# Kernel tuning notes

Hardware: AMD Instinct MI355X
Metric: run time of the kernel (lower is better)

The kernel has to match this reference:

```python
import jax, jax.numpy as jnp
import numpy as np

DIM = 10  # GMM components == feature dim


def _conv(x, w, b):
    y = jax.lax.conv_general_dilated(x, w, window_strides=(1, 1), padding='VALID',
                                     dimension_numbers=('NCHW', 'OIHW', 'NCHW'))
    return y + b[None, :, None, None]


def _gmm(x, centers, raw_mats):
    # x: [B, d]; centers: [K, d]; raw_mats: [K, d, d] with K == d == DIM
    K, d = centers.shape
    I = jnp.eye(d, dtype=x.dtype)
    L = jnp.tril(raw_mats, -1) + I                       # unit lower-triangular [K,d,d]
    root_D = jnp.diagonal(raw_mats, axis1=-2, axis2=-1)  # [K,d]
    D = root_D * root_D + 1e-4
    # Sigma_inv = L^{-T} D^{-1} L^{-1}
    L_inv = jax.scipy.linalg.solve_triangular(L, jnp.broadcast_to(I, L.shape), lower=True)
    Sigma_inv = jnp.einsum('kai,ka,kaj->kij', L_inv, 1.0 / D, L_inv)
    det_scale = jax.lax.rsqrt(jnp.prod(D, axis=-1))      # [K]
    diff = x[:, None, :] - centers[None, :, :]           # [B,K,d]
    dist_sq = jnp.einsum('bkd,kde,bke->bk', diff, Sigma_inv, diff)
    expo = -0.5 * dist_sq
    expo_safe = expo - jnp.max(expo, axis=1, keepdims=True)
    numer = det_scale[None, :] * jnp.exp(expo_safe)
    return numer / jnp.sum(numer, axis=1, keepdims=True)


def setup_inputs() -> dict:
    key = jax.random.key(0)
    ks = jax.random.split(key, 12)
    B = 4096
    x = jax.random.normal(ks[0], (B, 1, 28, 28), dtype=jnp.float32)
    conv1_w = jax.random.normal(ks[1], (32, 1, 3, 3), jnp.float32) * (1.0 / np.sqrt(1 * 9))
    conv1_b = jnp.zeros((32,), jnp.float32)
    conv2_w = jax.random.normal(ks[2], (64, 32, 3, 3), jnp.float32) * (1.0 / np.sqrt(32 * 9))
    conv2_b = jnp.zeros((64,), jnp.float32)
    fc1_w = jax.random.normal(ks[3], (128, 9216), jnp.float32) * (1.0 / np.sqrt(9216))
    fc1_b = jnp.zeros((128,), jnp.float32)
    fc2_w = jax.random.normal(ks[4], (DIM, 128), jnp.float32) * (1.0 / np.sqrt(128))
    fc2_b = jnp.zeros((DIM,), jnp.float32)
    centers = jax.random.normal(ks[5], (DIM, DIM), jnp.float32)
    raw_mats = jax.random.normal(ks[6], (DIM, DIM, DIM), jnp.float32) * 0.1 + jnp.eye(DIM)[None]
    return {'x': x, 'conv1_w': conv1_w, 'conv1_b': conv1_b, 'conv2_w': conv2_w,
            'conv2_b': conv2_b, 'fc1_w': fc1_w, 'fc1_b': fc1_b, 'fc2_w': fc2_w,
            'fc2_b': fc2_b, 'centers': centers, 'raw_mats': raw_mats}


def reference(x, conv1_w, conv1_b, conv2_w, conv2_b, fc1_w, fc1_b, fc2_w, fc2_b, centers, raw_mats):
    h = jax.nn.relu(_conv(x, conv1_w, conv1_b))          # [B,32,26,26]
    h = jax.nn.relu(_conv(h, conv2_w, conv2_b))          # [B,64,24,24]
    h = jax.lax.reduce_window(h, -jnp.inf, jax.lax.max, (1, 1, 2, 2), (1, 1, 2, 2), 'VALID')
    h = h.reshape(h.shape[0], -1)                        # [B,9216] (dropout = identity in eval)
    h = jax.nn.relu(h @ fc1_w.T + fc1_b)
    h = h @ fc2_w.T + fc2_b                              # [B,10]
    return _gmm(h, centers, raw_mats)
```

## Files before the change

### kernel.cpp

```cpp
#include <hip/hip_runtime.h>

typedef _Float16 half_t;
typedef _Float16 half8  __attribute__((ext_vector_type(8)));
typedef _Float16 half2v __attribute__((ext_vector_type(2)));
typedef float    floatx4 __attribute__((ext_vector_type(4)));

#define MFMA16(a, b, c) __builtin_amdgcn_mfma_f32_16x16x32_f16((a), (b), (c), 0, 0, 0)

__global__ void k_prep(const float* __restrict__ fw1, half_t* __restrict__ W1h,
                       const float* __restrict__ w2, half_t* __restrict__ W2T,
                       const float* __restrict__ raw, float* __restrict__ Sinv,
                       float* __restrict__ dets) {
    const int blk = blockIdx.x;
    const int t = threadIdx.x;
    if (blk < 4608) {
        const int i = blk * 256 + t;
        W1h[i] = (half_t)fw1[i];
    } else if (blk < 4680) {
        const int i = (blk - 4608) * 256 + t;
        if (i < 18432) {
            const int tap = i / 2048;
            const int r = i - tap * 2048;
            const int co = r >> 5;
            const int ci = r & 31;
            W2T[i] = (half_t)w2[(co * 32 + ci) * 9 + tap];
        }
    } else if (t < 10) {
        const float* R = raw + t * 100;
        float Rr[100];
#pragma unroll
        for (int i = 0; i < 100; ++i) Rr[i] = R[i];
        float Li[10][10];
#pragma unroll
        for (int j = 0; j < 10; ++j) {
#pragma unroll
            for (int i = 0; i < 10; ++i) Li[i][j] = (i == j) ? 1.0f : 0.0f;
#pragma unroll
            for (int i = 1; i < 10; ++i) {
                if (i > j) {
                    float s = 0.0f;
#pragma unroll
                    for (int m = 0; m < 10; ++m)
                        if (m >= j && m < i) s -= Rr[i * 10 + m] * Li[m][j];
                    Li[i][j] = s;
                }
            }
        }
        float Dl[10];
        float prod = 1.0f;
#pragma unroll
        for (int a = 0; a < 10; ++a) {
            float rd = Rr[a * 10 + a];
            float dv = rd * rd + 1e-4f;
            Dl[a] = 1.0f / dv;
            prod *= dv;
        }
        dets[t] = rsqrtf(prod);
#pragma unroll
        for (int i = 0; i < 10; ++i)
#pragma unroll
            for (int j = 0; j < 10; ++j) {
                float s = 0.0f;
#pragma unroll
                for (int a = 0; a < 10; ++a) s += Li[a][i] * Dl[a] * Li[a][j];
                Sinv[t * 100 + i * 10 + j] = s;
            }
    }
}

__global__ __launch_bounds__(256, 2) void k_convs(
    const float* __restrict__ x, const float* __restrict__ w1,
    const float* __restrict__ b1, const float* __restrict__ b2,
    const half_t* __restrict__ W2T, half_t* __restrict__ h2p) {
    __shared__ float s_x[784];
    __shared__ float s_w1[288];
    __shared__ float s_b1[32];
    __shared__ float s_b2[64];
    __shared__ __align__(16) half_t s_h1[4][26][26][8];

    const int t = threadIdx.x;
    const int b = blockIdx.x;

    for (int i = t; i < 784; i += 256) s_x[i] = x[(size_t)b * 784 + i];
    for (int i = t; i < 288; i += 256) s_w1[i] = w1[i];
    if (t < 32) s_b1[t] = b1[t];
    if (t < 64) s_b2[t] = b2[t];
    __syncthreads();

    const int w = t >> 6;
    const int ln = t & 63;
    const int n16 = ln & 15;
    const int q = ln >> 4;

    {
        float wr[8][9], br[8];
#pragma unroll
        for (int j = 0; j < 8; ++j) {
            br[j] = s_b1[w * 8 + j];
#pragma unroll
            for (int k = 0; k < 9; ++k) wr[j][k] = s_w1[(w * 8 + j) * 9 + k];
        }
        for (int p = ln; p < 676; p += 64) {
            const int yy = p / 26;
            const int xx = p - yy * 26;
            float win[9];
#pragma unroll
            for (int r = 0; r < 3; ++r)
#pragma unroll
                for (int c = 0; c < 3; ++c) win[r * 3 + c] = s_x[(yy + r) * 28 + xx + c];
            half8 hv;
#pragma unroll
            for (int j = 0; j < 8; ++j) {
                float a = br[j];
#pragma unroll
                for (int k = 0; k < 9; ++k) a = fmaf(win[k], wr[j][k], a);
                hv[j] = (half_t)fmaxf(a, 0.0f);
            }
            *(half8*)(&s_h1[w][yy][xx][0]) = hv;
        }
    }

    half8 bf[9][4];
#pragma unroll
    for (int tap = 0; tap < 9; ++tap)
#pragma unroll
        for (int ct = 0; ct < 4; ++ct)
            bf[tap][ct] = *(const half8*)(W2T + ((tap * 64 + ct * 16 + n16) * 32 + q * 8));

    __syncthreads();

#pragma unroll
    for (int tap = 0; tap < 9; ++tap)
#pragma unroll
        for (int ct = 0; ct < 4; ++ct)
            asm volatile("" : "+v"(bf[tap][ct]));

    const int dy = (ln >> 3) & 1;
    const int dx = ln & 7;

    for (int i = 0; i < 9; ++i) {
        const int mt = w * 9 + i;
        const int ty = mt / 3;
        const int tx = mt - ty * 3;
        const int y0 = 2 * ty, x0 = 8 * tx;
        floatx4 acc[4];
#pragma unroll
        for (int ct = 0; ct < 4; ++ct) acc[ct] = (floatx4){0.f, 0.f, 0.f, 0.f};
#pragma unroll
        for (int tap = 0; tap < 9; ++tap) {
            const int ky = tap / 3;
            const int kx = tap - ky * 3;
            half8 af = *(const half8*)(&s_h1[q][y0 + dy + ky][x0 + dx + kx][0]);
#pragma unroll
            for (int ct = 0; ct < 4; ++ct) acc[ct] = MFMA16(af, bf[tap][ct], acc[ct]);
        }
#pragma unroll
        for (int ct = 0; ct < 4; ++ct) {
            float p0 = fmaxf(acc[ct][0], acc[ct][1]);
            float p1 = fmaxf(acc[ct][2], acc[ct][3]);
            p0 = fmaxf(p0, __shfl_xor(p0, 32, 64));
            p1 = fmaxf(p1, __shfl_xor(p1, 32, 64));
            if (q < 2) {
                const int co = ct * 16 + n16;
                const float bb = s_b2[co];
                half2v hz;
                hz[0] = (half_t)fmaxf(p0 + bb, 0.0f);
                hz[1] = (half_t)fmaxf(p1 + bb, 0.0f);
                *(half2v*)(h2p + (size_t)b * 9216 + co * 144 + ty * 12 + 4 * tx + 2 * q) = hz;
            }
        }
    }
}

__global__ __launch_bounds__(256) void k_fc1(const half_t* __restrict__ A,
                                             const half_t* __restrict__ W,
                                             half_t* __restrict__ part) {
    const int t = threadIdx.x;
    const int mb = blockIdx.x;
    const int kb = blockIdx.y;
    const int w = t >> 6, ln = t & 63, n16 = ln & 15, q = ln >> 4;

    const half_t* a0 = A + (size_t)(mb * 128 + w * 32 + n16) * 9216 + kb * 576 + q * 8;
    const half_t* a1 = a0 + (size_t)16 * 9216;
    const half_t* wp = W + (size_t)n16 * 9216 + kb * 576 + q * 8;

    floatx4 acc[2][8];
#pragma unroll
    for (int s = 0; s < 2; ++s)
#pragma unroll
        for (int nt = 0; nt < 8; ++nt) acc[s][nt] = (floatx4){0.f, 0.f, 0.f, 0.f};

    for (int kt = 0; kt < 18; ++kt) {
        const int ko = kt * 32;
        half8 af0 = *(const half8*)(a0 + ko);
        half8 af1 = *(const half8*)(a1 + ko);
#pragma unroll
        for (int nt = 0; nt < 8; ++nt) {
            half8 bfr = *(const half8*)(wp + (size_t)nt * 16 * 9216 + ko);
            acc[0][nt] = MFMA16(af0, bfr, acc[0][nt]);
            acc[1][nt] = MFMA16(af1, bfr, acc[1][nt]);
        }
    }
    const int rowbase = mb * 128 + w * 32;
#pragma unroll
    for (int s = 0; s < 2; ++s)
#pragma unroll
        for (int nt = 0; nt < 8; ++nt)
#pragma unroll
            for (int r = 0; r < 4; ++r) {
                const int row = rowbase + s * 16 + q * 4 + r;
                const int col = nt * 16 + n16;
                part[(size_t)kb * 524288 + (size_t)row * 128 + col] = (half_t)acc[s][nt][r];
            }
}

__global__ void k_fc1red(const half_t* __restrict__ part, const float* __restrict__ b,
                         half_t* __restrict__ h3) {
    const int idx = blockIdx.x * 256 + threadIdx.x;
    const int col = idx & 127;
    float s = 0.0f;
#pragma unroll
    for (int j = 0; j < 16; ++j) s += (float)part[(size_t)j * 524288 + idx];
    s = fmaxf(s + b[col], 0.0f);
    h3[idx] = (half_t)s;
}

__global__ __launch_bounds__(256) void k_fc2gmm(
    const half_t* __restrict__ h3, const float* __restrict__ fw,
    const float* __restrict__ fb, const float* __restrict__ cent,
    const float* __restrict__ Sinv, const float* __restrict__ dets,
    float* __restrict__ out) {
    __shared__ float sw[1280];
    __shared__ float sb[10];
    __shared__ float sc[100];
    __shared__ float ss[1000];
    __shared__ float sd[10];
    const int t = threadIdx.x;
    for (int i = t; i < 1280; i += 256) sw[i] = fw[i];
    if (t < 10) sb[t] = fb[t];
    if (t < 100) sc[t] = cent[t];
    for (int i = t; i < 1000; i += 256) ss[i] = Sinv[i];
    if (t < 10) sd[t] = dets[t];
    __syncthreads();

    const int bidx = blockIdx.x * 256 + t;
    half2v hh[64];
    const half2v* hp = (const half2v*)(h3 + (size_t)bidx * 128);
#pragma unroll
    for (int i = 0; i < 64; ++i) hh[i] = hp[i];

    float y[10];
#pragma unroll
    for (int o = 0; o < 10; ++o) {
        float a = sb[o];
#pragma unroll
        for (int k = 0; k < 64; ++k) {
            a = fmaf((float)hh[k][0], sw[o * 128 + 2 * k], a);
            a = fmaf((float)hh[k][1], sw[o * 128 + 2 * k + 1], a);
        }
        y[o] = a;
    }

    float expo[10];
    float mx = -3.402823466e38f;
#pragma unroll
    for (int k = 0; k < 10; ++k) {
        float d[10];
#pragma unroll
        for (int j = 0; j < 10; ++j) d[j] = y[j] - sc[k * 10 + j];
        float s = 0.0f;
#pragma unroll
        for (int i = 0; i < 10; ++i) {
            float r = 0.0f;
#pragma unroll
            for (int j = 0; j < 10; ++j) r = fmaf(ss[k * 100 + i * 10 + j], d[j], r);
            s = fmaf(d[i], r, s);
        }
        expo[k] = -0.5f * s;
        mx = fmaxf(mx, expo[k]);
    }
    float num[10];
    float sum = 0.0f;
#pragma unroll
    for (int k = 0; k < 10; ++k) {
        num[k] = sd[k] * __expf(expo[k] - mx);
        sum += num[k];
    }
    const float inv = 1.0f / sum;
#pragma unroll
    for (int k = 0; k < 10; ++k) out[(size_t)bidx * 10 + k] = num[k] * inv;
}

extern "C" void kernel_launch(void* const* d_in, const int* in_sizes, int n_in,
                              void* d_out, int out_size, void* d_ws, size_t ws_size,
                              hipStream_t stream) {
    const float* x = (const float*)d_in[0];
    const float* w1 = (const float*)d_in[1];
    const float* b1 = (const float*)d_in[2];
    const float* w2 = (const float*)d_in[3];
    const float* b2 = (const float*)d_in[4];
    const float* fw1 = (const float*)d_in[5];
    const float* fb1 = (const float*)d_in[6];
    const float* fw2 = (const float*)d_in[7];
    const float* fb2 = (const float*)d_in[8];
    const float* cen = (const float*)d_in[9];
    const float* raw = (const float*)d_in[10];
    float* out = (float*)d_out;

    char* ws = (char*)d_ws;
    half_t* W2T = (half_t*)(ws);
    half_t* W1h = (half_t*)(ws + 36864);
    half_t* h2p = (half_t*)(ws + 2396160);
    half_t* part = (half_t*)(ws + 77893632);
    half_t* h3h = (half_t*)(ws + 94670848);
    float* gS = (float*)(ws + 95719424);
    float* gD = (float*)(ws + 95723424);

    k_prep<<<4681, 256, 0, stream>>>(fw1, W1h, w2, W2T, raw, gS, gD);
    k_convs<<<4096, 256, 0, stream>>>(x, w1, b1, b2, W2T, h2p);
    k_fc1<<<dim3(32, 16), 256, 0, stream>>>(h2p, W1h, part);
    k_fc1red<<<2048, 256, 0, stream>>>(part, fb1, h3h);
    k_fc2gmm<<<16, 256, 0, stream>>>(h3h, fw2, fb2, cen, gS, gD, out);
}
```

Baseline: 283.6 us.

## Warp-specialize conv kernel into producer/consumer pipeline over 8 images per block

The fused conv kernel becomes a persistent-style kernel with 512 threads and 8 images per block. Four waves compute conv1 into a double-buffered shared tile while four other waves run the MFMA conv2 and pool on the previous image. Weights are loaded once per block instead of once per image, and conv1 for the next image overlaps conv2 for the current one. In exchange the grid shrinks to 512 blocks, which may underfill the GPU's CUs. The pipeline also runs one extra stage, and the two wave groups may be unbalanced, leaving one group idle at each barrier.

```diff
diff --git a/kernel.cpp b/kernel.cpp
--- a/kernel.cpp
+++ b/kernel.cpp
@@ -68,107 +68,112 @@
     }
 }
 
-__global__ __launch_bounds__(256, 2) void k_convs(
+__global__ __launch_bounds__(512, 2) void k_convs(
     const float* __restrict__ x, const float* __restrict__ w1,
     const float* __restrict__ b1, const float* __restrict__ b2,
     const half_t* __restrict__ W2T, half_t* __restrict__ h2p) {
-    __shared__ float s_x[784];
-    __shared__ float s_w1[288];
-    __shared__ float s_b1[32];
-    __shared__ float s_b2[64];
-    __shared__ __align__(16) half_t s_h1[4][26][26][8];
+    __shared__ float s_x[2][784];
+    __shared__ __align__(16) half_t s_h1[2][4][26][26][8];
 
     const int t = threadIdx.x;
-    const int b = blockIdx.x;
-
-    for (int i = t; i < 784; i += 256) s_x[i] = x[(size_t)b * 784 + i];
-    for (int i = t; i < 288; i += 256) s_w1[i] = w1[i];
-    if (t < 32) s_b1[t] = b1[t];
-    if (t < 64) s_b2[t] = b2[t];
-    __syncthreads();
-
     const int w = t >> 6;
     const int ln = t & 63;
+    const size_t base_img = (size_t)blockIdx.x * 8;
+
+    float wr[8][9], br[8];
+    half8 bf[9][4];
+    float bb[4];
     const int n16 = ln & 15;
     const int q = ln >> 4;
-
-    {
-        float wr[8][9], br[8];
-#pragma unroll
-        for (int j = 0; j < 8; ++j) {
-            br[j] = s_b1[w * 8 + j];
-#pragma unroll
-            for (int k = 0; k < 9; ++k) wr[j][k] = s_w1[(w * 8 + j) * 9 + k];
-        }
-        for (int p = ln; p < 676; p += 64) {
-            const int yy = p / 26;
-            const int xx = p - yy * 26;
-            float win[9];
-#pragma unroll
-            for (int r = 0; r < 3; ++r)
-#pragma unroll
-                for (int c = 0; c < 3; ++c) win[r * 3 + c] = s_x[(yy + r) * 28 + xx + c];
-            half8 hv;
-#pragma unroll
-            for (int j = 0; j < 8; ++j) {
-                float a = br[j];
-#pragma unroll
-                for (int k = 0; k < 9; ++k) a = fmaf(win[k], wr[j][k], a);
-                hv[j] = (half_t)fmaxf(a, 0.0f);
-            }
-            *(half8*)(&s_h1[w][yy][xx][0]) = hv;
-        }
-    }
-
-    half8 bf[9][4];
-#pragma unroll
-    for (int tap = 0; tap < 9; ++tap)
-#pragma unroll
-        for (int ct = 0; ct < 4; ++ct)
-            bf[tap][ct] = *(const half8*)(W2T + ((tap * 64 + ct * 16 + n16) * 32 + q * 8));
-
-    __syncthreads();
-
-#pragma unroll
-    for (int tap = 0; tap < 9; ++tap)
-#pragma unroll
-        for (int ct = 0; ct < 4; ++ct)
-            asm volatile("" : "+v"(bf[tap][ct]));
-
     const int dy = (ln >> 3) & 1;
     const int dx = ln & 7;
 
-    for (int i = 0; i < 9; ++i) {
-        const int mt = w * 9 + i;
-        const int ty = mt / 3;
-        const int tx = mt - ty * 3;
-        const int y0 = 2 * ty, x0 = 8 * tx;
-        floatx4 acc[4];
-#pragma unroll
-        for (int ct = 0; ct < 4; ++ct) acc[ct] = (floatx4){0.f, 0.f, 0.f, 0.f};
-#pragma unroll
-        for (int tap = 0; tap < 9; ++tap) {
-            const int ky = tap / 3;
-            const int kx = tap - ky * 3;
-            half8 af = *(const half8*)(&s_h1[q][y0 + dy + ky][x0 + dx + kx][0]);
-#pragma unroll
-            for (int ct = 0; ct < 4; ++ct) acc[ct] = MFMA16(af, bf[tap][ct], acc[ct]);
-        }
-#pragma unroll
-        for (int ct = 0; ct < 4; ++ct) {
-            float p0 = fmaxf(acc[ct][0], acc[ct][1]);
-            float p1 = fmaxf(acc[ct][2], acc[ct][3]);
-            p0 = fmaxf(p0, __shfl_xor(p0, 32, 64));
-            p1 = fmaxf(p1, __shfl_xor(p1, 32, 64));
-            if (q < 2) {
-                const int co = ct * 16 + n16;
-                const float bb = s_b2[co];
-                half2v hz;
-                hz[0] = (half_t)fmaxf(p0 + bb, 0.0f);
-                hz[1] = (half_t)fmaxf(p1 + bb, 0.0f);
-                *(half2v*)(h2p + (size_t)b * 9216 + co * 144 + ty * 12 + 4 * tx + 2 * q) = hz;
-            }
-        }
+    if (w < 4) {
+#pragma unroll
+        for (int j = 0; j < 8; ++j) {
+            br[j] = b1[w * 8 + j];
+#pragma unroll
+            for (int k = 0; k < 9; ++k) wr[j][k] = w1[(w * 8 + j) * 9 + k];
+        }
+        for (int i = t; i < 784; i += 256) s_x[0][i] = x[base_img * 784 + i];
+    } else {
+#pragma unroll
+        for (int tap = 0; tap < 9; ++tap)
+#pragma unroll
+            for (int ct = 0; ct < 4; ++ct)
+                bf[tap][ct] = *(const half8*)(W2T + ((tap * 64 + ct * 16 + n16) * 32 + q * 8));
+#pragma unroll
+        for (int ct = 0; ct < 4; ++ct) bb[ct] = b2[ct * 16 + n16];
+    }
+    __syncthreads();
+
+    for (int it = 0; it < 9; ++it) {
+        if (w < 4) {
+            if (it < 8) {
+                if (it + 1 < 8) {
+                    const float* xp = x + (base_img + it + 1) * 784;
+                    for (int i = t; i < 784; i += 256) s_x[(it + 1) & 1][i] = xp[i];
+                }
+                const float* sx = s_x[it & 1];
+                half_t* h1o = &s_h1[it & 1][w][0][0][0];
+                for (int p = ln; p < 676; p += 64) {
+                    const int yy = p / 26;
+                    const int xx = p - yy * 26;
+                    float win[9];
+#pragma unroll
+                    for (int r = 0; r < 3; ++r)
+#pragma unroll
+                        for (int c = 0; c < 3; ++c) win[r * 3 + c] = sx[(yy + r) * 28 + xx + c];
+                    half8 hv;
+#pragma unroll
+                    for (int j = 0; j < 8; ++j) {
+                        float a = br[j];
+#pragma unroll
+                        for (int k = 0; k < 9; ++k) a = fmaf(win[k], wr[j][k], a);
+                        hv[j] = (half_t)fmaxf(a, 0.0f);
+                    }
+                    *(half8*)(h1o + (yy * 26 + xx) * 8) = hv;
+                }
+            }
+        } else {
+            if (it >= 1) {
+                const int cw = w - 4;
+                const size_t img = base_img + it - 1;
+                const half_t* h1i = &s_h1[(it - 1) & 1][q][0][0][0];
+                for (int i = 0; i < 9; ++i) {
+                    const int mt = cw * 9 + i;
+                    const int ty = mt / 3;
+                    const int tx = mt - ty * 3;
+                    const int y0 = 2 * ty, x0 = 8 * tx;
+                    floatx4 acc[4];
+#pragma unroll
+                    for (int ct = 0; ct < 4; ++ct) acc[ct] = (floatx4){0.f, 0.f, 0.f, 0.f};
+#pragma unroll
+                    for (int tap = 0; tap < 9; ++tap) {
+                        const int ky = tap / 3;
+                        const int kx = tap - ky * 3;
+                        half8 af = *(const half8*)(h1i + (((y0 + dy + ky) * 26) + (x0 + dx + kx)) * 8);
+#pragma unroll
+                        for (int ct = 0; ct < 4; ++ct) acc[ct] = MFMA16(af, bf[tap][ct], acc[ct]);
+                    }
+#pragma unroll
+                    for (int ct = 0; ct < 4; ++ct) {
+                        float p0 = fmaxf(acc[ct][0], acc[ct][1]);
+                        float p1 = fmaxf(acc[ct][2], acc[ct][3]);
+                        p0 = fmaxf(p0, __shfl_xor(p0, 32, 64));
+                        p1 = fmaxf(p1, __shfl_xor(p1, 32, 64));
+                        if (q < 2) {
+                            const int co = ct * 16 + n16;
+                            half2v hz;
+                            hz[0] = (half_t)fmaxf(p0 + bb[ct], 0.0f);
+                            hz[1] = (half_t)fmaxf(p1 + bb[ct], 0.0f);
+                            *(half2v*)(h2p + img * 9216 + co * 144 + ty * 12 + 4 * tx + 2 * q) = hz;
+                        }
+                    }
+                }
+            }
+        }
+        __syncthreads();
     }
 }
 
@@ -317,7 +322,7 @@
     float* gD = (float*)(ws + 95723424);
 
     k_prep<<<4681, 256, 0, stream>>>(fw1, W1h, w2, W2T, raw, gS, gD);
-    k_convs<<<4096, 256, 0, stream>>>(x, w1, b1, b2, W2T, h2p);
+    k_convs<<<512, 512, 0, stream>>>(x, w1, b1, b2, W2T, h2p);
     k_fc1<<<dim3(32, 16), 256, 0, stream>>>(h2p, W1h, part);
     k_fc1red<<<2048, 256, 0, stream>>>(part, fb1, h3h);
     k_fc2gmm<<<16, 256, 0, stream>>>(h3h, fw2, fb2, cen, gS, gD, out);
```

Result: slower. 345.7 us (+21.9%).
